# Kernel optimization log

Measured on AMD Instinct MI355X. Metric: run time of the kernel, lower is better.

The kernel has to match this reference:

```python
import jax, jax.numpy as jnp
import numpy as np

DIM = 1024
N_HEADS = 16
HEAD_DIM = DIM // N_HEADS
B, S = 2, 2048
NEG = -1e9  # additive causal mask value (finite, safe in low precision)


def setup_inputs() -> dict:
    key = jax.random.key(0)
    k_x, k_q, k_k, k_v, k_o = jax.random.split(key, 5)
    x = jax.random.normal(k_x, (B, S, DIM), dtype=jnp.float32)
    # causal additive mask, broadcastable to [B, H, S, S]
    causal = jnp.triu(jnp.ones((S, S), dtype=bool), k=1)
    mask = jnp.where(causal, NEG, 0.0).astype(jnp.float32)[None, None]
    scale = 1.0 / np.sqrt(DIM)
    wq = jax.random.normal(k_q, (DIM, DIM), dtype=jnp.float32) * scale
    wk = jax.random.normal(k_k, (DIM, DIM), dtype=jnp.float32) * scale
    wv = jax.random.normal(k_v, (DIM, DIM), dtype=jnp.float32) * scale
    wo = jax.random.normal(k_o, (DIM, DIM), dtype=jnp.float32) * scale
    return {"x": x, "mask": mask, "wq": wq, "wk": wk, "wv": wv, "wo": wo}


def reference(x, mask, wq, wk, wv, wo):
    bs, seqlen, _ = x.shape
    # nn.Linear(y) = y @ W^T ; weights stored as (out, in)
    q = (x @ wq.T).reshape(bs, seqlen, N_HEADS, HEAD_DIM)
    k = (x @ wk.T).reshape(bs, seqlen, N_HEADS, HEAD_DIM)
    v = (x @ wv.T).reshape(bs, seqlen, N_HEADS, HEAD_DIM)
    # scores: [B, H, S, S] — intentionally materialized, as in the original
    attn = jnp.einsum('bqhd,bkhd->bhqk', q, k) / np.sqrt(HEAD_DIM)
    attn = attn + mask
    attn = jax.nn.softmax(attn, axis=-1)
    out = jnp.einsum('bhqk,bkhd->bqhd', attn, v).reshape(bs, seqlen, DIM)
    return out @ wo.T
```

## Files before the change

kernel.cpp:

```cpp
#include <hip/hip_runtime.h>

typedef __attribute__((ext_vector_type(8))) short bf16x8;
typedef __attribute__((ext_vector_type(4))) float f32x4;
typedef __attribute__((ext_vector_type(16))) float f32x16;
typedef __attribute__((ext_vector_type(4))) unsigned short u16x4;
typedef __attribute__((ext_vector_type(8))) unsigned short u16x8;

#define DIM 1024
#define SEQ 2048
#define NHEAD 16
#define HDIM 64
#define C2 0.18033688011112042f

#define WAIT_VM4() asm volatile("s_waitcnt vmcnt(4)" ::: "memory")
#define WAIT_VM3() asm volatile("s_waitcnt vmcnt(3)" ::: "memory")
#define WAIT_VM0() asm volatile("s_waitcnt vmcnt(0)" ::: "memory")
#define BAR() __builtin_amdgcn_s_barrier()
#define SCHEDB() __builtin_amdgcn_sched_barrier(0)

__device__ __forceinline__ unsigned short f2bf(float f) {
  union { float f; unsigned u; } v; v.f = f;
  unsigned r = v.u + 0x7fffu + ((v.u >> 16) & 1u);
  return (unsigned short)(r >> 16);
}

__device__ __forceinline__ float bf2f(unsigned short s) {
  union { unsigned u; float f; } v; v.u = ((unsigned)s) << 16;
  return v.f;
}

__device__ __forceinline__ void gload_lds16(const void* g, void* l) {
  __builtin_amdgcn_global_load_lds(
      (const __attribute__((address_space(1))) void*)g,
      (__attribute__((address_space(3))) void*)l, 16, 0, 0);
}

__device__ __forceinline__ f32x16 mfma32(bf16x8 a, bf16x8 b, f32x16 c) {
  return __builtin_amdgcn_mfma_f32_32x32x16_bf16(a, b, c, 0, 0, 0);
}

__device__ __forceinline__ unsigned cvtpk(float lo, float hi) {
  unsigned r;
  asm("v_cvt_pk_bf16_f32 %0, %1, %2" : "=v"(r) : "v"(lo), "v"(hi));
  return r;
}

__global__ void f2bf_all(const float* __restrict__ x, const float* __restrict__ wq,
                         const float* __restrict__ wk, const float* __restrict__ wv,
                         const float* __restrict__ wo, unsigned short* __restrict__ xb,
                         unsigned short* __restrict__ wb) {
  int blk = blockIdx.x;
  const float* src;
  unsigned short* dst;
  int rb;
  if (blk < 4096) { src = x; dst = xb; rb = blk; }
  else {
    int w = (blk - 4096) >> 10;
    src = w == 0 ? wq : w == 1 ? wk : w == 2 ? wv : wo;
    dst = wb + (size_t)w * 1048576;
    rb = (blk - 4096) & 1023;
  }
  int i = rb * 256 + threadIdx.x;
  float4 v = ((const float4*)src)[i];
  u16x4 o;
  o[0] = f2bf(v.x); o[1] = f2bf(v.y); o[2] = f2bf(v.z); o[3] = f2bf(v.w);
  ((u16x4*)dst)[i] = o;
}

__global__ __launch_bounds__(256) void gemm3(
    const unsigned short* __restrict__ xb,
    const unsigned short* __restrict__ wb,
    unsigned short* __restrict__ qkv) {
  __shared__ unsigned short As[2][4096];
  __shared__ unsigned short Bs[2][4096];
  const int bz = blockIdx.x;
  const unsigned short *A, *B;
  unsigned short* C;
  int m0, n0, ldc;
  float cscale = 1.0f;
  if (bz < 512) {
    int xcd = bz & 7, inner = bz >> 3;
    int mm = inner & 3, n = (inner >> 2) & 7, w = inner >> 5;
    m0 = (xcd * 4 + mm) * 128; n0 = n * 128;
    A = xb; B = wb + w * 1048576; C = qkv + w * 4194304; ldc = 1024;
    if (w == 0) cscale = C2;
  } else {
    int idx = bz - 512;
    int xcd = idx & 7, inner = idx >> 3;
    int tt = inner & 3, mv = inner >> 2;
    m0 = mv * 128; n0 = (xcd * 4 + tt) * 128;
    A = wb + 2 * 1048576; B = xb; C = qkv + 2 * 4194304; ldc = 4096;
  }
  const int tid = threadIdx.x;
  const int wv = tid >> 6, lane = tid & 63;
  const int g = lane >> 4, l16 = lane & 15;
  const int wm = (wv >> 1) * 64, wn = (wv & 1) * 64;
  const int sro = lane >> 2, sc4 = lane & 3;
  f32x4 acc[4][4] = {};

  const int rA0 = wv * 32 + sro, rA1 = wv * 32 + 16 + sro;
  const int cd0 = (sc4 ^ ((rA0 >> 1) & 3)) * 8, cd1 = (sc4 ^ ((rA1 >> 1) & 3)) * 8;
  const unsigned short* Ap0 = A + (long long)(m0 + rA0) * 1024 + cd0;
  const unsigned short* Ap1 = A + (long long)(m0 + rA1) * 1024 + cd1;
  const unsigned short* Bp0 = B + (long long)(n0 + rA0) * 1024 + cd0;
  const unsigned short* Bp1 = B + (long long)(n0 + rA1) * 1024 + cd1;

#define GSTAGE(BUF)                                                            \
  {                                                                            \
    gload_lds16(Ap0, &As[BUF][wv * 1024]);                                     \
    gload_lds16(Ap1, &As[BUF][wv * 1024 + 512]);                               \
    gload_lds16(Bp0, &Bs[BUF][wv * 1024]);                                     \
    gload_lds16(Bp1, &Bs[BUF][wv * 1024 + 512]);                               \
    Ap0 += 32; Ap1 += 32; Bp0 += 32; Bp1 += 32;                                \
  }

  GSTAGE(0);
  GSTAGE(1);

  for (int it = 0; it < 32; ++it) {
    const int buf = it & 1;
    WAIT_VM4();
    BAR();
    SCHEDB();
    bf16x8 af[4], bfr[4];
#pragma unroll
    for (int mf = 0; mf < 4; ++mf) {
      int row = wm + mf * 16 + l16;
      af[mf] = *(const bf16x8*)((const char*)&As[buf][0] + row * 64 +
                                ((g ^ ((row >> 1) & 3)) << 4));
    }
#pragma unroll
    for (int nf = 0; nf < 4; ++nf) {
      int row = wn + nf * 16 + l16;
      bfr[nf] = *(const bf16x8*)((const char*)&Bs[buf][0] + row * 64 +
                                 ((g ^ ((row >> 1) & 3)) << 4));
    }
#pragma unroll
    for (int mf = 0; mf < 4; ++mf)
#pragma unroll
      for (int nf = 0; nf < 4; ++nf)
        acc[mf][nf] = __builtin_amdgcn_mfma_f32_16x16x32_bf16(
            af[mf], bfr[nf], acc[mf][nf], 0, 0, 0);
    SCHEDB();
    BAR();
    if (it + 1 < 32) GSTAGE(buf);
  }

#pragma unroll
  for (int mf = 0; mf < 4; ++mf)
#pragma unroll
    for (int nf = 0; nf < 4; ++nf)
#pragma unroll
      for (int r = 0; r < 4; ++r) {
        long long m = m0 + wm + mf * 16 + g * 4 + r;
        long long n = n0 + wn + nf * 16 + l16;
        C[m * ldc + n] = f2bf(acc[mf][nf][r] * cscale);
      }
}

__global__ __launch_bounds__(256) void gemm_out(
    const unsigned short* __restrict__ A,
    const unsigned short* __restrict__ B,
    float* __restrict__ C) {
  __shared__ unsigned short As[2][2048];
  __shared__ unsigned short Bs[2][4096];
  const int tid = threadIdx.x;
  const int wv = tid >> 6, lane = tid & 63;
  const int g = lane >> 4, l16 = lane & 15;
  const int m0 = blockIdx.y * 64, n0 = blockIdx.x * 128;
  const int wm = (wv >> 1) * 32, wn = (wv & 1) * 64;
  const int sro = lane >> 2, sc4 = lane & 3;
  f32x4 acc[2][4] = {};

  const int rA = wv * 16 + sro;
  const int rB0 = wv * 32 + sro, rB1 = wv * 32 + 16 + sro;
  const int cdA = (sc4 ^ ((rA >> 1) & 3)) * 8;
  const int cdB0 = (sc4 ^ ((rB0 >> 1) & 3)) * 8, cdB1 = (sc4 ^ ((rB1 >> 1) & 3)) * 8;
  const unsigned short* Ap = A + (long long)(m0 + rA) * 1024 + cdA;
  const unsigned short* Bp0 = B + (long long)(n0 + rB0) * 1024 + cdB0;
  const unsigned short* Bp1 = B + (long long)(n0 + rB1) * 1024 + cdB1;

#define OSTAGE(BUF)                                                            \
  {                                                                            \
    gload_lds16(Ap, &As[BUF][wv * 512]);                                       \
    gload_lds16(Bp0, &Bs[BUF][wv * 1024]);                                     \
    gload_lds16(Bp1, &Bs[BUF][wv * 1024 + 512]);                               \
    Ap += 32; Bp0 += 32; Bp1 += 32;                                            \
  }

  OSTAGE(0);
  OSTAGE(1);

  for (int it = 0; it < 32; ++it) {
    const int buf = it & 1;
    WAIT_VM3();
    BAR();
    SCHEDB();
    bf16x8 af[2], bfr[4];
#pragma unroll
    for (int mf = 0; mf < 2; ++mf) {
      int row = wm + mf * 16 + l16;
      af[mf] = *(const bf16x8*)((const char*)&As[buf][0] + row * 64 +
                                ((g ^ ((row >> 1) & 3)) << 4));
    }
#pragma unroll
    for (int nf = 0; nf < 4; ++nf) {
      int row = wn + nf * 16 + l16;
      bfr[nf] = *(const bf16x8*)((const char*)&Bs[buf][0] + row * 64 +
                                 ((g ^ ((row >> 1) & 3)) << 4));
    }
#pragma unroll
    for (int mf = 0; mf < 2; ++mf)
#pragma unroll
      for (int nf = 0; nf < 4; ++nf)
        acc[mf][nf] = __builtin_amdgcn_mfma_f32_16x16x32_bf16(
            af[mf], bfr[nf], acc[mf][nf], 0, 0, 0);
    SCHEDB();
    BAR();
    if (it + 1 < 32) OSTAGE(buf);
  }

#pragma unroll
  for (int mf = 0; mf < 2; ++mf)
#pragma unroll
    for (int nf = 0; nf < 4; ++nf)
#pragma unroll
      for (int r = 0; r < 4; ++r) {
        long long m = m0 + wm + mf * 16 + g * 4 + r;
        long long n = n0 + wn + nf * 16 + l16;
        C[m * 1024 + n] = acc[mf][nf][r];
      }
}

__global__ __launch_bounds__(256, 4) void attn_kernel(
    const unsigned short* __restrict__ Qg,
    const unsigned short* __restrict__ Kg,
    const unsigned short* __restrict__ VTg,
    unsigned short* __restrict__ Og,
    unsigned short* __restrict__ pacc,
    float* __restrict__ pml) {
  __shared__ unsigned short Kls[2][4096];
  __shared__ unsigned short Vls[2][4096];

  const int tid = threadIdx.x;
  const int wv = tid >> 6, lane = tid & 63;
  const int l32 = lane & 31, hi = lane >> 5;
  const int h = blockIdx.y, b = blockIdx.z;

  const int i = blockIdx.x;
  int qt, c, cn;
  if (i < 16)      { qt = 15 - (i >> 2); c = i & 3; cn = 4; }
  else if (i < 28) { int j = i - 16; qt = 11 - j / 3; c = j % 3; cn = 3; }
  else if (i < 36) { int j = i - 28; qt = 7 - ((j >> 1)); c = j & 1; cn = 2; }
  else             { qt = 39 - i; c = 0; cn = 1; }

  const int nt = 2 * qt + 2;
  const int t0 = c * 8;
  const int tb = min(t0 + 8, nt);
  const int umax = 4 * qt + wv;

  const int q = qt * 128 + wv * 32 + l32;
  const long long bh = (long long)b * SEQ * DIM + h * HDIM;
  const long long vbase = (long long)h * HDIM * 4096 + b * SEQ;

  const unsigned short* Qrow = Qg + (long long)(b * SEQ + q) * DIM + h * HDIM;
  bf16x8 qf[4];
#pragma unroll
  for (int ds = 0; ds < 4; ++ds)
    qf[ds] = *(const bf16x8*)(Qrow + ds * 16 + hi * 8);
  WAIT_VM0();

  bf16x8 ones;
#pragma unroll
  for (int j = 0; j < 8; ++j) ones[j] = (short)0x3F80;

  f32x16 acc0 = {}, acc1 = {}, lacc = {};

  const int xm = l32 & 7;
  int cb4_0 = ((0 | hi) ^ xm) * 16;
  int cb4_1 = ((2 | hi) ^ xm) * 16;
  int cb4_2 = ((4 | hi) ^ xm) * 16;
  int cb4_3 = ((6 | hi) ^ xm) * 16;
  const int krb = l32 * 128;

  const int sr = lane >> 3, sc = lane & 7;
  const int r0 = wv * 16 + sr, r1 = wv * 16 + 8 + sr;
  const int cs0 = (sc ^ (r0 & 7)) * 8, cs1 = (sc ^ (r1 & 7)) * 8;
  const unsigned short* Kp0 = Kg + bh + (long long)(t0 * 64 + r0) * DIM + cs0;
  const unsigned short* Kp1 = Kg + bh + (long long)(t0 * 64 + r1) * DIM + cs1;
  const unsigned short* Vp0 = VTg + vbase + (long long)r0 * 4096 + t0 * 64 + cs0;
  const unsigned short* Vp1 = VTg + vbase + (long long)r1 * 4096 + t0 * 64 + cs1;
  const int ld0 = (wv * 16) * 64 + sr * 0;

#define STAGE(BUF)                                                             \
  {                                                                            \
    gload_lds16(Kp0, &Kls[BUF][wv * 1024]);                                    \
    gload_lds16(Kp1, &Kls[BUF][wv * 1024 + 512]);                              \
    gload_lds16(Vp0, &Vls[BUF][wv * 1024]);                                    \
    gload_lds16(Vp1, &Vls[BUF][wv * 1024 + 512]);                              \
    Kp0 += 64 * 1024; Kp1 += 64 * 1024; Vp0 += 64; Vp1 += 64;                  \
  }

  STAGE(0);
  STAGE(1);

  for (int t = t0; t < tb; ++t) {
    const int buf = (t - t0) & 1;
    WAIT_VM4();
    BAR();
    SCHEDB();

#pragma unroll
    for (int s = 0; s < 2; ++s) {
      const int u = 2 * t + s;
      if (u <= umax) {
        const char* Kb = (const char*)&Kls[buf][0] + s * 4096 + krb;
        f32x16 sv = {};
        __builtin_amdgcn_s_setprio(1);
        sv = mfma32(*(const bf16x8*)(Kb + cb4_0), qf[0], sv);
        sv = mfma32(*(const bf16x8*)(Kb + cb4_1), qf[1], sv);
        sv = mfma32(*(const bf16x8*)(Kb + cb4_2), qf[2], sv);
        sv = mfma32(*(const bf16x8*)(Kb + cb4_3), qf[3], sv);
        __builtin_amdgcn_s_setprio(0);

        if (u == umax) {
#pragma unroll
          for (int r = 0; r < 16; ++r) {
            int kw = (r & 3) + 8 * (r >> 2) + 4 * hi;
            if (kw > l32) sv[r] = -1e30f;
          }
        }

#pragma unroll
        for (int r = 0; r < 16; ++r) sv[r] = __builtin_amdgcn_exp2f(sv[r]);

        const char* Vb0 = (const char*)&Vls[buf][0] + krb;
        const char* Vb1 = Vb0 + 32 * 128;
        __builtin_amdgcn_s_setprio(1);
#pragma unroll
        for (int kk = 0; kk < 2; ++kk) {
          const int base = kk * 8;
          unsigned a0 = cvtpk(sv[base + 0], sv[base + 1]);
          unsigned a1 = cvtpk(sv[base + 2], sv[base + 3]);
          unsigned a2 = cvtpk(sv[base + 4], sv[base + 5]);
          unsigned a3 = cvtpk(sv[base + 6], sv[base + 7]);
          asm("v_permlane32_swap_b32 %0, %1" : "+v"(a0), "+v"(a2));
          asm("v_permlane32_swap_b32 %0, %1" : "+v"(a1), "+v"(a3));
          union { unsigned u4[4]; bf16x8 v; } pf;
          pf.u4[0] = a0; pf.u4[1] = a1; pf.u4[2] = a2; pf.u4[3] = a3;
          const int cbv = (2 * s + kk) == 0 ? cb4_0 : (2 * s + kk) == 1 ? cb4_1
                        : (2 * s + kk) == 2 ? cb4_2 : cb4_3;
          acc0 = mfma32(*(const bf16x8*)(Vb0 + cbv), pf.v, acc0);
          acc1 = mfma32(*(const bf16x8*)(Vb1 + cbv), pf.v, acc1);
          lacc = mfma32(ones, pf.v, lacc);
        }
        __builtin_amdgcn_s_setprio(0);
      }
    }
    SCHEDB();
    BAR();
    if (t + 1 < tb) STAGE(buf);
  }

  const float l_run = lacc[0];

  if (cn == 1) {
    const float inv_l = 1.0f / l_run;
    unsigned short* Orow = Og + (long long)(b * SEQ + q) * DIM + h * HDIM;
#pragma unroll
    for (int dblk = 0; dblk < 2; ++dblk) {
#pragma unroll
      for (int g4 = 0; g4 < 4; ++g4) {
        float v0 = (dblk ? acc1[g4 * 4 + 0] : acc0[g4 * 4 + 0]) * inv_l;
        float v1 = (dblk ? acc1[g4 * 4 + 1] : acc0[g4 * 4 + 1]) * inv_l;
        float v2 = (dblk ? acc1[g4 * 4 + 2] : acc0[g4 * 4 + 2]) * inv_l;
        float v3 = (dblk ? acc1[g4 * 4 + 3] : acc0[g4 * 4 + 3]) * inv_l;
        union { unsigned u[2]; u16x4 v; } o;
        o.u[0] = cvtpk(v0, v1);
        o.u[1] = cvtpk(v2, v3);
        *(u16x4*)(Orow + dblk * 32 + 8 * g4 + 4 * hi) = o.v;
      }
    }
  } else {
    const int sbase = qt < 8 ? 2 * (qt - 4) : qt < 12 ? 8 + 3 * (qt - 8) : 20 + 4 * (qt - 12);
    const int slot = (b * NHEAD + h) * 36 + sbase + c;
    unsigned short* pbase = pacc + (size_t)slot * 8192 + (wv * 32 + l32) * 64;
#pragma unroll
    for (int dblk = 0; dblk < 2; ++dblk) {
#pragma unroll
      for (int g4 = 0; g4 < 4; ++g4) {
        float v0 = dblk ? acc1[g4 * 4 + 0] : acc0[g4 * 4 + 0];
        float v1 = dblk ? acc1[g4 * 4 + 1] : acc0[g4 * 4 + 1];
        float v2 = dblk ? acc1[g4 * 4 + 2] : acc0[g4 * 4 + 2];
        float v3 = dblk ? acc1[g4 * 4 + 3] : acc0[g4 * 4 + 3];
        union { unsigned u[2]; u16x4 v; } o;
        o.u[0] = cvtpk(v0, v1);
        o.u[1] = cvtpk(v2, v3);
        *(u16x4*)(pbase + dblk * 32 + 8 * g4 + 4 * hi) = o.v;
      }
    }
    if (hi == 0) pml[slot * 128 + wv * 32 + l32] = l_run;
  }
}

__global__ __launch_bounds__(256) void attn_merge(
    const unsigned short* __restrict__ pacc,
    const float* __restrict__ pml,
    unsigned short* __restrict__ Og) {
  const int qt = 4 + blockIdx.x;
  const int h = blockIdx.y, b = blockIdx.z;
  const int cn = (qt >> 2) + 1;
  const int sbase = qt < 8 ? 2 * (qt - 4) : qt < 12 ? 8 + 3 * (qt - 8) : 20 + 4 * (qt - 12);
  const int base_slot = (b * NHEAD + h) * 36 + sbase;
  const int t = threadIdx.x;
  const int ql = t >> 1, d0 = (t & 1) * 32;

  float L = 0.f;
#pragma unroll
  for (int cc = 0; cc < 4; ++cc)
    if (cc < cn) L += pml[(base_slot + cc) * 128 + ql];
  const float invL = 1.0f / L;

  float o[32] = {};
#pragma unroll
  for (int cc = 0; cc < 4; ++cc)
    if (cc < cn) {
      const unsigned short* p = pacc + (size_t)(base_slot + cc) * 8192 + ql * 64 + d0;
#pragma unroll
      for (int k = 0; k < 32; k += 8) {
        u16x8 v = *(const u16x8*)(p + k);
#pragma unroll
        for (int jv = 0; jv < 8; ++jv) o[k + jv] += bf2f(v[jv]);
      }
    }

  const int q = qt * 128 + ql;
  unsigned short* orow = Og + (size_t)(b * SEQ + q) * DIM + h * HDIM + d0;
#pragma unroll
  for (int k = 0; k < 32; k += 8) {
    union { unsigned u[4]; u16x8 v; } ov;
#pragma unroll
    for (int jv = 0; jv < 4; ++jv)
      ov.u[jv] = cvtpk(o[k + 2 * jv] * invL, o[k + 2 * jv + 1] * invL);
    *(u16x8*)(orow + k) = ov.v;
  }
}

extern "C" void kernel_launch(void* const* d_in, const int* in_sizes, int n_in,
                              void* d_out, int out_size, void* d_ws, size_t ws_size,
                              hipStream_t stream) {
  const float* x   = (const float*)d_in[0];
  const float* wq  = (const float*)d_in[2];
  const float* wk  = (const float*)d_in[3];
  const float* wv_ = (const float*)d_in[4];
  const float* wo  = (const float*)d_in[5];

  unsigned short* xb  = (unsigned short*)d_ws;
  unsigned short* wb  = xb + (size_t)4096 * 1024;
  unsigned short* qkv = wb + (size_t)4 * 1024 * 1024;
  unsigned short* ao  = qkv + (size_t)3 * 4096 * 1024;
  unsigned short* pacc = ao + (size_t)4096 * 1024;
  float* pml = (float*)(pacc + (size_t)1152 * 8192);

  f2bf_all<<<8192, 256, 0, stream>>>(x, wq, wk, wv_, wo, xb, wb);

  gemm3<<<768, 256, 0, stream>>>(xb, wb, qkv);

  attn_kernel<<<dim3(40, 16, 2), 256, 0, stream>>>(
      qkv, qkv + 4194304, qkv + 2 * 4194304, ao, pacc, pml);

  attn_merge<<<dim3(12, 16, 2), 256, 0, stream>>>(pacc, pml, ao);

  gemm_out<<<dim3(8, 64), 256, 0, stream>>>(ao, wb + 3145728, (float*)d_out);
}
```

Measured before the change: 110.3 us.

## Widen attention blocks to 256 queries with 8 waves sharing K/V tiles

```diff
diff --git a/kernel.cpp b/kernel.cpp
--- a/kernel.cpp
+++ b/kernel.cpp
@@ -14,6 +14,7 @@
 
 #define WAIT_VM4() asm volatile("s_waitcnt vmcnt(4)" ::: "memory")
 #define WAIT_VM3() asm volatile("s_waitcnt vmcnt(3)" ::: "memory")
+#define WAIT_VM2() asm volatile("s_waitcnt vmcnt(2)" ::: "memory")
 #define WAIT_VM0() asm volatile("s_waitcnt vmcnt(0)" ::: "memory")
 #define BAR() __builtin_amdgcn_s_barrier()
 #define SCHEDB() __builtin_amdgcn_sched_barrier(0)
@@ -232,7 +233,7 @@
       }
 }
 
-__global__ __launch_bounds__(256, 4) void attn_kernel(
+__global__ __launch_bounds__(512, 4) void attn_kernel(
     const unsigned short* __restrict__ Qg,
     const unsigned short* __restrict__ Kg,
     const unsigned short* __restrict__ VTg,
@@ -248,18 +249,26 @@
   const int h = blockIdx.y, b = blockIdx.z;
 
   const int i = blockIdx.x;
-  int qt, c, cn;
-  if (i < 16)      { qt = 15 - (i >> 2); c = i & 3; cn = 4; }
-  else if (i < 28) { int j = i - 16; qt = 11 - j / 3; c = j % 3; cn = 3; }
-  else if (i < 36) { int j = i - 28; qt = 7 - ((j >> 1)); c = j & 1; cn = 2; }
-  else             { qt = 39 - i; c = 0; cn = 1; }
-
-  const int nt = 2 * qt + 2;
+  int qt8, c;
+  if (i < 4)        { qt8 = 7; c = i; }
+  else if (i < 7)   { qt8 = 6; c = i - 4; }
+  else if (i < 10)  { qt8 = 5; c = i - 7; }
+  else if (i < 12)  { qt8 = 4; c = i - 10; }
+  else if (i < 14)  { qt8 = 3; c = i - 12; }
+  else if (i == 14) { qt8 = 2; c = 0; }
+  else if (i == 15) { qt8 = 1; c = 0; }
+  else if (i == 16) { qt8 = 6; c = 3; }
+  else if (i == 17) { qt8 = 4; c = 2; }
+  else if (i == 18) { qt8 = 2; c = 1; }
+  else              { qt8 = 0; c = 0; }
+  const int cn = (qt8 + 2) >> 1;
+
+  const int nt = 4 * qt8 + 4;
   const int t0 = c * 8;
   const int tb = min(t0 + 8, nt);
-  const int umax = 4 * qt + wv;
-
-  const int q = qt * 128 + wv * 32 + l32;
+  const int umax = 8 * qt8 + wv;
+
+  const int q = qt8 * 256 + wv * 32 + l32;
   const long long bh = (long long)b * SEQ * DIM + h * HDIM;
   const long long vbase = (long long)h * HDIM * 4096 + b * SEQ;
 
@@ -277,28 +286,23 @@
   f32x16 acc0 = {}, acc1 = {}, lacc = {};
 
   const int xm = l32 & 7;
-  int cb4_0 = ((0 | hi) ^ xm) * 16;
-  int cb4_1 = ((2 | hi) ^ xm) * 16;
-  int cb4_2 = ((4 | hi) ^ xm) * 16;
-  int cb4_3 = ((6 | hi) ^ xm) * 16;
+  const int cb4_0 = ((0 | hi) ^ xm) * 16;
+  const int cb4_1 = ((2 | hi) ^ xm) * 16;
+  const int cb4_2 = ((4 | hi) ^ xm) * 16;
+  const int cb4_3 = ((6 | hi) ^ xm) * 16;
   const int krb = l32 * 128;
 
   const int sr = lane >> 3, sc = lane & 7;
-  const int r0 = wv * 16 + sr, r1 = wv * 16 + 8 + sr;
-  const int cs0 = (sc ^ (r0 & 7)) * 8, cs1 = (sc ^ (r1 & 7)) * 8;
+  const int r0 = wv * 8 + sr;
+  const int cs0 = (sc ^ (r0 & 7)) * 8;
   const unsigned short* Kp0 = Kg + bh + (long long)(t0 * 64 + r0) * DIM + cs0;
-  const unsigned short* Kp1 = Kg + bh + (long long)(t0 * 64 + r1) * DIM + cs1;
   const unsigned short* Vp0 = VTg + vbase + (long long)r0 * 4096 + t0 * 64 + cs0;
-  const unsigned short* Vp1 = VTg + vbase + (long long)r1 * 4096 + t0 * 64 + cs1;
-  const int ld0 = (wv * 16) * 64 + sr * 0;
 
 #define STAGE(BUF)                                                             \
   {                                                                            \
-    gload_lds16(Kp0, &Kls[BUF][wv * 1024]);                                    \
-    gload_lds16(Kp1, &Kls[BUF][wv * 1024 + 512]);                              \
-    gload_lds16(Vp0, &Vls[BUF][wv * 1024]);                                    \
-    gload_lds16(Vp1, &Vls[BUF][wv * 1024 + 512]);                              \
-    Kp0 += 64 * 1024; Kp1 += 64 * 1024; Vp0 += 64; Vp1 += 64;                  \
+    gload_lds16(Kp0, &Kls[BUF][wv * 512]);                                     \
+    gload_lds16(Vp0, &Vls[BUF][wv * 512]);                                     \
+    Kp0 += 64 * 1024; Vp0 += 64;                                               \
   }
 
   STAGE(0);
@@ -306,7 +310,7 @@
 
   for (int t = t0; t < tb; ++t) {
     const int buf = (t - t0) & 1;
-    WAIT_VM4();
+    WAIT_VM2();
     BAR();
     SCHEDB();
 
@@ -382,9 +386,10 @@
       }
     }
   } else {
-    const int sbase = qt < 8 ? 2 * (qt - 4) : qt < 12 ? 8 + 3 * (qt - 8) : 20 + 4 * (qt - 12);
-    const int slot = (b * NHEAD + h) * 36 + sbase + c;
-    unsigned short* pbase = pacc + (size_t)slot * 8192 + (wv * 32 + l32) * 64;
+    const int sb = qt8 == 2 ? 0 : qt8 == 3 ? 2 : qt8 == 4 ? 4
+                 : qt8 == 5 ? 7 : qt8 == 6 ? 10 : 14;
+    const int slot = (b * NHEAD + h) * 18 + sb + c;
+    unsigned short* pbase = pacc + (size_t)slot * 16384 + (wv * 32 + l32) * 64;
 #pragma unroll
     for (int dblk = 0; dblk < 2; ++dblk) {
 #pragma unroll
@@ -399,7 +404,7 @@
         *(u16x4*)(pbase + dblk * 32 + 8 * g4 + 4 * hi) = o.v;
       }
     }
-    if (hi == 0) pml[slot * 128 + wv * 32 + l32] = l_run;
+    if (hi == 0) pml[slot * 256 + wv * 32 + l32] = l_run;
   }
 }
 
@@ -407,42 +412,49 @@
     const unsigned short* __restrict__ pacc,
     const float* __restrict__ pml,
     unsigned short* __restrict__ Og) {
-  const int qt = 4 + blockIdx.x;
+  const int qt8 = 2 + blockIdx.x;
   const int h = blockIdx.y, b = blockIdx.z;
-  const int cn = (qt >> 2) + 1;
-  const int sbase = qt < 8 ? 2 * (qt - 4) : qt < 12 ? 8 + 3 * (qt - 8) : 20 + 4 * (qt - 12);
-  const int base_slot = (b * NHEAD + h) * 36 + sbase;
+  const int cn = (qt8 + 2) >> 1;
+  const int sb = qt8 == 2 ? 0 : qt8 == 3 ? 2 : qt8 == 4 ? 4
+               : qt8 == 5 ? 7 : qt8 == 6 ? 10 : 14;
+  const int base_slot = (b * NHEAD + h) * 18 + sb;
   const int t = threadIdx.x;
-  const int ql = t >> 1, d0 = (t & 1) * 32;
-
-  float L = 0.f;
-#pragma unroll
-  for (int cc = 0; cc < 4; ++cc)
-    if (cc < cn) L += pml[(base_slot + cc) * 128 + ql];
-  const float invL = 1.0f / L;
-
-  float o[32] = {};
-#pragma unroll
-  for (int cc = 0; cc < 4; ++cc)
-    if (cc < cn) {
-      const unsigned short* p = pacc + (size_t)(base_slot + cc) * 8192 + ql * 64 + d0;
-#pragma unroll
-      for (int k = 0; k < 32; k += 8) {
-        u16x8 v = *(const u16x8*)(p + k);
-#pragma unroll
-        for (int jv = 0; jv < 8; ++jv) o[k + jv] += bf2f(v[jv]);
-      }
-    }
-
-  const int q = qt * 128 + ql;
-  unsigned short* orow = Og + (size_t)(b * SEQ + q) * DIM + h * HDIM + d0;
-#pragma unroll
-  for (int k = 0; k < 32; k += 8) {
-    union { unsigned u[4]; u16x8 v; } ov;
-#pragma unroll
-    for (int jv = 0; jv < 4; ++jv)
-      ov.u[jv] = cvtpk(o[k + 2 * jv] * invL, o[k + 2 * jv + 1] * invL);
-    *(u16x8*)(orow + k) = ov.v;
+
+#pragma unroll
+  for (int rr = 0; rr < 2; ++rr) {
+    const int row = rr * 128 + (t >> 1);
+    const int d0 = (t & 1) * 32;
+
+    float L = 0.f;
+#pragma unroll
+    for (int cc = 0; cc < 4; ++cc)
+      if (cc < cn) L += pml[(base_slot + cc) * 256 + row];
+    const float invL = 1.0f / L;
+
+    float o[32] = {};
+#pragma unroll
+    for (int cc = 0; cc < 4; ++cc)
+      if (cc < cn) {
+        const unsigned short* p =
+            pacc + (size_t)(base_slot + cc) * 16384 + (size_t)row * 64 + d0;
+#pragma unroll
+        for (int k = 0; k < 32; k += 8) {
+          u16x8 v = *(const u16x8*)(p + k);
+#pragma unroll
+          for (int jv = 0; jv < 8; ++jv) o[k + jv] += bf2f(v[jv]);
+        }
+      }
+
+    const int q = qt8 * 256 + row;
+    unsigned short* orow = Og + (size_t)(b * SEQ + q) * DIM + h * HDIM + d0;
+#pragma unroll
+    for (int k = 0; k < 32; k += 8) {
+      union { unsigned u[4]; u16x8 v; } ov;
+#pragma unroll
+      for (int jv = 0; jv < 4; ++jv)
+        ov.u[jv] = cvtpk(o[k + 2 * jv] * invL, o[k + 2 * jv + 1] * invL);
+      *(u16x8*)(orow + k) = ov.v;
+    }
   }
 }
 
@@ -460,16 +472,16 @@
   unsigned short* qkv = wb + (size_t)4 * 1024 * 1024;
   unsigned short* ao  = qkv + (size_t)3 * 4096 * 1024;
   unsigned short* pacc = ao + (size_t)4096 * 1024;
-  float* pml = (float*)(pacc + (size_t)1152 * 8192);
+  float* pml = (float*)(pacc + (size_t)576 * 16384);
 
   f2bf_all<<<8192, 256, 0, stream>>>(x, wq, wk, wv_, wo, xb, wb);
 
   gemm3<<<768, 256, 0, stream>>>(xb, wb, qkv);
 
-  attn_kernel<<<dim3(40, 16, 2), 256, 0, stream>>>(
+  attn_kernel<<<dim3(20, 16, 2), 512, 0, stream>>>(
       qkv, qkv + 4194304, qkv + 2 * 4194304, ao, pacc, pml);
 
-  attn_merge<<<dim3(12, 16, 2), 256, 0, stream>>>(pacc, pml, ao);
+  attn_merge<<<dim3(6, 16, 2), 256, 0, stream>>>(pacc, pml, ao);
 
   gemm_out<<<dim3(8, 64), 256, 0, stream>>>(ao, wb + 3145728, (float*)d_out);
 }
```

Result: slower. 114.8 us (+4.0%).
